# Kernel optimization log

Hardware: AMD Instinct MI355X
Metric: run time of the kernel (lower is better)

The kernel has to match this reference:

```python
import jax, jax.numpy as jnp
from jax import lax
import numpy as np

B, L = 16, 256
CHAR_SIZE, WORD_SIZE = 8000, 50000
EMB = 128            # char_embed (shared by char and word embeddings)
ENT_NUM, ENT_EMB = 30, 64
REL = 64             # rel_num
H = 10               # LSTM hidden (hard-coded in the source)


def lstm(x, mask, Wx, Wh, b, reverse=False):
    """Keras-style masked LSTM, return_sequences=True. x: [B,L,D], mask: [B,L] bool."""
    if reverse:
        x, mask = x[:, ::-1], mask[:, ::-1]
    gates_x = x @ Wx + b  # [B,L,4H] precomputed input projection

    def step(carry, inp):
        h, c = carry
        gx, m = inp  # gx: [B,4H], m: [B]
        z = gx + h @ Wh
        i, f, g, o = jnp.split(z, 4, axis=-1)  # keras gate order i,f,c,o
        i, f, o = jax.nn.sigmoid(i), jax.nn.sigmoid(f), jax.nn.sigmoid(o)
        c_new = f * c + i * jnp.tanh(g)
        h_new = o * jnp.tanh(c_new)
        m = m[:, None]
        h2 = jnp.where(m, h_new, h)  # masked steps carry previous state/output
        c2 = jnp.where(m, c_new, c)
        return (h2, c2), h2

    h0 = jnp.zeros((x.shape[0], Wh.shape[0]), x.dtype)
    _, hs = lax.scan(step, (h0, h0), (gates_x.transpose(1, 0, 2), mask.T))
    hs = hs.transpose(1, 0, 2)  # [B,L,H]
    if reverse:
        hs = hs[:, ::-1]
    return hs


def setup_inputs() -> dict:
    key = jax.random.key(0)
    ks = jax.random.split(key, 24)
    dense = lambda k, i, o: (0.05 * jax.random.normal(k, (i, o), jnp.float32))
    inp = {}
    inp["char_ids"] = jax.random.randint(ks[0], (B, L), 1, CHAR_SIZE, dtype=jnp.int32)
    inp["word_ids"] = jax.random.randint(ks[1], (B, L), 0, WORD_SIZE, dtype=jnp.int32)
    inp["entity_ids"] = jax.random.randint(ks[2], (B, L), 0, ENT_NUM, dtype=jnp.int32)
    inp["char_table"] = 0.05 * jax.random.normal(ks[3], (CHAR_SIZE, EMB), jnp.float32)
    inp["word_table"] = 0.05 * jax.random.normal(ks[4], (WORD_SIZE, EMB), jnp.float32)
    inp["ent_table"] = 0.05 * jax.random.normal(ks[5], (ENT_NUM, ENT_EMB), jnp.float32)
    D = 2 * EMB
    inp["Wx_f"], inp["Wh_f"], inp["b_f"] = dense(ks[6], D, 4 * H), dense(ks[7], H, 4 * H), jnp.zeros((4 * H,), jnp.float32)
    inp["Wx_b"], inp["Wh_b"], inp["b_b"] = dense(ks[8], D, 4 * H), dense(ks[9], H, 4 * H), jnp.zeros((4 * H,), jnp.float32)
    inp["We"], inp["be"] = dense(ks[10], 2 * H, ENT_NUM), jnp.zeros((ENT_NUM,), jnp.float32)
    ENC = 2 * H + ENT_EMB
    inp["Wu"], inp["bu"] = dense(ks[11], ENC, REL), jnp.zeros((REL,), jnp.float32)
    inp["Wv"], inp["bv"] = dense(ks[12], ENC, REL), jnp.zeros((REL,), jnp.float32)
    inp["Wuv"], inp["buv"] = dense(ks[13], 2 * REL, REL), jnp.zeros((REL,), jnp.float32)
    inp["Wr"], inp["br"] = dense(ks[14], REL, REL), jnp.zeros((REL,), jnp.float32)
    return inp


def reference(char_ids, word_ids, entity_ids, char_table, word_table, ent_table,
              Wx_f, Wh_f, b_f, Wx_b, Wh_b, b_b, We, be,
              Wu, bu, Wv, bv, Wuv, buv, Wr, br):
    mask = char_ids != 0  # [B,L]
    embed = jnp.concatenate([char_table[char_ids], word_table[word_ids]], axis=-1)  # [B,L,2E]
    h_fwd = lstm(embed, mask, Wx_f, Wh_f, b_f, reverse=False)
    h_bwd = lstm(embed, mask, Wx_b, Wh_b, b_b, reverse=True)
    sent = jnp.concatenate([h_fwd, h_bwd], axis=-1)  # [B,L,20]
    entity_logits = sent @ We + be  # [B,L,ENT_NUM]
    # training=True path: use gold entity_ids
    rel_enc = jnp.concatenate([sent, ent_table[entity_ids]], axis=-1)  # [B,L,ENC]
    su = jax.nn.relu(rel_enc @ Wu + bu)  # [B,L,REL]  (relu(tile(u)) == tile(relu(u)))
    sv = jax.nn.relu(rel_enc @ Wv + bv)  # [B,L,REL]
    # Dense over concat([u_tiled, v_tiled]) == split-weight matmul + broadcast add:
    # uv[b,i,j] = relu(su[b,j]) @ Wuv[:REL] + relu(sv[b,i]) @ Wuv[REL:] + buv
    A = jnp.einsum('bjr,rk->bjk', su, Wuv[:REL])  # depends on j (axis 2)
    C = jnp.einsum('bir,rk->bik', sv, Wuv[REL:])  # depends on i (axis 1)
    uv = A[:, None, :, :] + C[:, :, None, :] + buv  # [B,L,L,REL]
    rel_logits = jax.nn.softmax(uv @ Wr + br, axis=-1)  # [B,L,L,REL]
    return entity_logits, rel_logits
```

## Files before the change

kernel.cpp:

```cpp
#include <hip/hip_runtime.h>
#include <hip/hip_bf16.h>

#define Bb 16
#define Ll 256
#define EMBd 128
#define Hh 10
#define G4 40
#define ENTN 30
#define ENCd 84

__device__ __forceinline__ float ex2(float x){ return __builtin_amdgcn_exp2f(x); }
__device__ __forceinline__ float frcp(float x){ return __builtin_amdgcn_rcpf(x); }
#define LOG2E 1.4426950408889634f
__device__ __forceinline__ float sigf(float x){ return frcp(1.f + ex2(-LOG2E*x)); }
__device__ __forceinline__ float tanhf_fast(float x){ return 1.f - 2.f*frcp(1.f + ex2(2.f*LOG2E*x)); }

__global__ __launch_bounds__(256) void k0_weights(
    const float* __restrict__ Wuv, const float* __restrict__ buv,
    const float* __restrict__ Wr,  const float* __restrict__ br,
    float* __restrict__ W1, float* __restrict__ W2, float* __restrict__ biasp) {
  int idx = blockIdx.x*256 + threadIdx.x;
  if (idx < 4096) {
    int r = idx >> 6, k = idx & 63;
    float acc = 0.f;
    #pragma unroll 8
    for (int s = 0; s < 64; ++s) acc = fmaf(Wuv[r*64+s], Wr[s*64+k], acc);
    W1[idx] = acc;
  } else if (idx < 8192) {
    int j = idx - 4096; int r = j >> 6, k = j & 63;
    float acc = 0.f;
    #pragma unroll 8
    for (int s = 0; s < 64; ++s) acc = fmaf(Wuv[(64+r)*64+s], Wr[s*64+k], acc);
    W2[j] = acc;
  } else if (idx < 8256) {
    int k = idx - 8192;
    float acc = br[k];
    #pragma unroll 8
    for (int s = 0; s < 64; ++s) acc = fmaf(buv[s], Wr[s*64+k], acc);
    biasp[k] = acc;
  }
}

__global__ __launch_bounds__(128) void k1_embed_gates(
    const int* __restrict__ char_ids, const int* __restrict__ word_ids,
    const float* __restrict__ char_table, const float* __restrict__ word_table,
    const float* __restrict__ Wx_f, const float* __restrict__ b_f,
    const float* __restrict__ Wx_b, const float* __restrict__ b_b,
    float* __restrict__ gx_f, float* __restrict__ gx_b) {
  int tok = blockIdx.x;
  int b = tok >> 8, t = tok & 255;
  int tid = threadIdx.x;
  __shared__ float e[256];
  int cid = char_ids[tok];
  int wid = word_ids[tok];
  e[tid]       = char_table[cid*EMBd + tid];
  e[tid + 128] = word_table[wid*EMBd + tid];
  __syncthreads();
  if (tid < G4) {
    float acc = b_f[tid];
    #pragma unroll 8
    for (int k = 0; k < 256; ++k) acc = fmaf(e[k], Wx_f[k*G4 + tid], acc);
    gx_f[(t*Bb + b)*G4 + tid] = acc;
  } else if (tid >= 64 && tid < 64 + G4) {
    int u = tid - 64;
    float acc = b_b[u];
    #pragma unroll 8
    for (int k = 0; k < 256; ++k) acc = fmaf(e[k], Wx_b[k*G4 + u], acc);
    gx_b[((Ll-1-t)*Bb + b)*G4 + u] = acc;
  }
}

__global__ __launch_bounds__(64) void k2_lstm(
    const int* __restrict__ char_ids,
    const float* __restrict__ gx_f, const float* __restrict__ gx_b,
    const float* __restrict__ Wh_f, const float* __restrict__ Wh_b,
    float* __restrict__ sent) {
  int bid = blockIdx.x;
  int dir = bid & 1, b = bid >> 1;
  int lane = threadIdx.x;
  int j = lane < Hh ? lane : 0;
  const float* gx = dir ? gx_b : gx_f;
  const float* Wh = dir ? Wh_b : Wh_f;
  float wA[Hh], wB[Hh], wC[Hh], wD[Hh];
  #pragma unroll
  for (int k = 0; k < Hh; ++k) {
    wA[k] = Wh[k*G4 + j];
    wB[k] = Wh[k*G4 + j + Hh];
    wC[k] = Wh[k*G4 + j + 2*Hh];
    wD[k] = Wh[k*G4 + j + 3*Hh];
  }
  float hbc[Hh];
  #pragma unroll
  for (int k = 0; k < Hh; ++k) hbc[k] = 0.f;
  float c = 0.f, h = 0.f;
  const float* gp = gx + b*G4 + j;
  float nI = gp[0], nF = gp[Hh], nG = gp[2*Hh], nO = gp[3*Hh];
  int ncid = char_ids[b*Ll + (dir ? Ll-1 : 0)];
  for (int t = 0; t < Ll; ++t) {
    float gI = nI, gF = nF, gG = nG, gO = nO;
    int cid = ncid;
    if (t < Ll-1) {
      const float* gn = gp + (size_t)(t+1)*Bb*G4;
      nI = gn[0]; nF = gn[Hh]; nG = gn[2*Hh]; nO = gn[3*Hh];
      ncid = char_ids[b*Ll + (dir ? (Ll-2-t) : (t+1))];
    }
    float zi = gI, zf = gF, zg = gG, zo = gO;
    #pragma unroll
    for (int k = 0; k < Hh; ++k) {
      zi = fmaf(hbc[k], wA[k], zi);
      zf = fmaf(hbc[k], wB[k], zf);
      zg = fmaf(hbc[k], wC[k], zg);
      zo = fmaf(hbc[k], wD[k], zo);
    }
    float ig = sigf(zi), fg = sigf(zf), og = sigf(zo);
    float gg = tanhf_fast(zg);
    float cn = fmaf(fg, c, ig*gg);
    float hn = og * tanhf_fast(cn);
    bool m = (cid != 0);
    c = m ? cn : c;
    h = m ? hn : h;
    int t_orig = dir ? (Ll-1-t) : t;
    if (lane < Hh) sent[(b*Ll + t_orig)*20 + dir*Hh + lane] = h;
    #pragma unroll
    for (int k = 0; k < Hh; ++k)
      hbc[k] = __uint_as_float(__builtin_amdgcn_readlane(__float_as_uint(h), k));
  }
}

__global__ __launch_bounds__(64) void k3_token(
    const int* __restrict__ entity_ids,
    const float* __restrict__ ent_table,
    const float* __restrict__ sent,
    const float* __restrict__ We, const float* __restrict__ be,
    const float* __restrict__ Wu, const float* __restrict__ bu,
    const float* __restrict__ Wv, const float* __restrict__ bv,
    const float* __restrict__ W1, const float* __restrict__ W2,
    float* __restrict__ ent_logits, float* __restrict__ Ap, float* __restrict__ Cp) {
  int tok = blockIdx.x;
  int tid = threadIdx.x;
  __shared__ float enc[ENCd];
  __shared__ float su[64], sv[64];
  int eid = entity_ids[tok];
  if (tid < 20) enc[tid] = sent[tok*20 + tid];
  if (tid < ENCd - 20) enc[20 + tid] = ent_table[eid*64 + tid];
  __syncthreads();
  float a = bu[tid], v = bv[tid];
  #pragma unroll 4
  for (int k = 0; k < ENCd; ++k) {
    float ek = enc[k];
    a = fmaf(ek, Wu[k*64 + tid], a);
    v = fmaf(ek, Wv[k*64 + tid], v);
  }
  a = fmaxf(a, 0.f); v = fmaxf(v, 0.f);
  su[tid] = a; sv[tid] = v;
  if (tid < ENTN) {
    float el = be[tid];
    #pragma unroll
    for (int k = 0; k < 20; ++k) el = fmaf(enc[k], We[k*ENTN + tid], el);
    ent_logits[tok*ENTN + tid] = el;
  }
  __syncthreads();
  float accA = 0.f, accC = 0.f;
  #pragma unroll 8
  for (int r = 0; r < 64; ++r) {
    accA = fmaf(su[r], W1[r*64 + tid], accA);
    accC = fmaf(sv[r], W2[r*64 + tid], accC);
  }
  Ap[tok*64 + tid] = accA;
  Cp[tok*64 + tid] = accC;
}

__global__ __launch_bounds__(256) void k4_rel(
    const float* __restrict__ Ap, const float* __restrict__ Cp,
    const float* __restrict__ biasp, float* __restrict__ rel) {
  int tid = threadIdx.x;
  int rowLocal = tid >> 4;
  int k4 = tid & 15;
  int row = blockIdx.x*16 + rowLocal;
  int b  = row >> 16;
  int ij = row & 65535;
  int i  = ij >> 8, j = ij & 255;
  const float4 a4 = *(const float4*)(Ap + ((size_t)(b*Ll + j))*64 + k4*4);
  const float4 c4 = *(const float4*)(Cp + ((size_t)(b*Ll + i))*64 + k4*4);
  const float4 bb = *(const float4*)(biasp + k4*4);
  float x0 = a4.x + c4.x + bb.x;
  float x1 = a4.y + c4.y + bb.y;
  float x2 = a4.z + c4.z + bb.z;
  float x3 = a4.w + c4.w + bb.w;
  float m = fmaxf(fmaxf(x0, x1), fmaxf(x2, x3));
  #pragma unroll
  for (int s = 1; s < 16; s <<= 1) m = fmaxf(m, __shfl_xor(m, s));
  float e0 = ex2(LOG2E*(x0 - m));
  float e1 = ex2(LOG2E*(x1 - m));
  float e2 = ex2(LOG2E*(x2 - m));
  float e3 = ex2(LOG2E*(x3 - m));
  float ssum = (e0 + e1) + (e2 + e3);
  #pragma unroll
  for (int s = 1; s < 16; s <<= 1) ssum += __shfl_xor(ssum, s);
  float rs = frcp(ssum);
  float4 o; o.x = e0*rs; o.y = e1*rs; o.z = e2*rs; o.w = e3*rs;
  *(float4*)(rel + (size_t)row*64 + k4*4) = o;
}

extern "C" void kernel_launch(void* const* d_in, const int* in_sizes, int n_in,
                              void* d_out, int out_size, void* d_ws, size_t ws_size,
                              hipStream_t stream) {
  const int*   char_ids   = (const int*)  d_in[0];
  const int*   word_ids   = (const int*)  d_in[1];
  const int*   entity_ids = (const int*)  d_in[2];
  const float* char_table = (const float*)d_in[3];
  const float* word_table = (const float*)d_in[4];
  const float* ent_table  = (const float*)d_in[5];
  const float* Wx_f = (const float*)d_in[6];
  const float* Wh_f = (const float*)d_in[7];
  const float* b_f  = (const float*)d_in[8];
  const float* Wx_b = (const float*)d_in[9];
  const float* Wh_b = (const float*)d_in[10];
  const float* b_b  = (const float*)d_in[11];
  const float* We = (const float*)d_in[12];
  const float* be = (const float*)d_in[13];
  const float* Wu = (const float*)d_in[14];
  const float* bu = (const float*)d_in[15];
  const float* Wv = (const float*)d_in[16];
  const float* bv = (const float*)d_in[17];
  const float* Wuv = (const float*)d_in[18];
  const float* buv = (const float*)d_in[19];
  const float* Wr  = (const float*)d_in[20];
  const float* br  = (const float*)d_in[21];

  float* ws   = (float*)d_ws;
  float* gx_f = ws;
  float* gx_b = gx_f + 163840;
  float* sent = gx_b + 163840;
  float* W1   = sent + 81920;
  float* W2   = W1 + 4096;
  float* biasp= W2 + 4096;
  float* Ap   = biasp + 64;
  float* Cp   = Ap + 262144;

  float* out = (float*)d_out;
  float* ent_logits = out;
  float* rel = out + 122880;

  hipLaunchKernelGGL(k0_weights, dim3(33), dim3(256), 0, stream,
                     Wuv, buv, Wr, br, W1, W2, biasp);
  hipLaunchKernelGGL(k1_embed_gates, dim3(4096), dim3(128), 0, stream,
                     char_ids, word_ids, char_table, word_table,
                     Wx_f, b_f, Wx_b, b_b, gx_f, gx_b);
  hipLaunchKernelGGL(k2_lstm, dim3(32), dim3(64), 0, stream,
                     char_ids, gx_f, gx_b, Wh_f, Wh_b, sent);
  hipLaunchKernelGGL(k3_token, dim3(4096), dim3(64), 0, stream,
                     entity_ids, ent_table, sent, We, be, Wu, bu, Wv, bv,
                     W1, W2, ent_logits, Ap, Cp);
  hipLaunchKernelGGL(k4_rel, dim3(65536), dim3(256), 0, stream, Ap, Cp, biasp, rel);
}
```

Before: 164.7 us.

## Fuse weight precompute into embed kernel, lane-per-gate LSTM, batched token kernel, nontemporal stores

The weight-folding kernel is merged into the embedding/gate kernel as extra blocks, which removes one launch. The LSTM recurrence now gives one lane to each of the 40 gate outputs, computes activations with a select-based formula, and gathers the gates with ds_bpermute, which shortens the per-step dependency chain. The token kernel stages Wu/Wv in shared memory and processes 16 tokens per 256-thread block. The rel softmax output uses nontemporal stores to avoid cache pollution on the large write.

```diff
diff --git a/kernel.cpp b/kernel.cpp
--- a/kernel.cpp
+++ b/kernel.cpp
@@ -9,48 +9,50 @@
 #define ENTN 30
 #define ENCd 84
 
+typedef float f32x4 __attribute__((ext_vector_type(4)));
+
 __device__ __forceinline__ float ex2(float x){ return __builtin_amdgcn_exp2f(x); }
 __device__ __forceinline__ float frcp(float x){ return __builtin_amdgcn_rcpf(x); }
 #define LOG2E 1.4426950408889634f
 __device__ __forceinline__ float sigf(float x){ return frcp(1.f + ex2(-LOG2E*x)); }
 __device__ __forceinline__ float tanhf_fast(float x){ return 1.f - 2.f*frcp(1.f + ex2(2.f*LOG2E*x)); }
 
-__global__ __launch_bounds__(256) void k0_weights(
-    const float* __restrict__ Wuv, const float* __restrict__ buv,
-    const float* __restrict__ Wr,  const float* __restrict__ br,
-    float* __restrict__ W1, float* __restrict__ W2, float* __restrict__ biasp) {
-  int idx = blockIdx.x*256 + threadIdx.x;
-  if (idx < 4096) {
-    int r = idx >> 6, k = idx & 63;
-    float acc = 0.f;
-    #pragma unroll 8
-    for (int s = 0; s < 64; ++s) acc = fmaf(Wuv[r*64+s], Wr[s*64+k], acc);
-    W1[idx] = acc;
-  } else if (idx < 8192) {
-    int j = idx - 4096; int r = j >> 6, k = j & 63;
-    float acc = 0.f;
-    #pragma unroll 8
-    for (int s = 0; s < 64; ++s) acc = fmaf(Wuv[(64+r)*64+s], Wr[s*64+k], acc);
-    W2[j] = acc;
-  } else if (idx < 8256) {
-    int k = idx - 8192;
-    float acc = br[k];
-    #pragma unroll 8
-    for (int s = 0; s < 64; ++s) acc = fmaf(buv[s], Wr[s*64+k], acc);
-    biasp[k] = acc;
-  }
-}
-
-__global__ __launch_bounds__(128) void k1_embed_gates(
+__global__ __launch_bounds__(128) void k01_embed_gates_weights(
     const int* __restrict__ char_ids, const int* __restrict__ word_ids,
     const float* __restrict__ char_table, const float* __restrict__ word_table,
     const float* __restrict__ Wx_f, const float* __restrict__ b_f,
     const float* __restrict__ Wx_b, const float* __restrict__ b_b,
-    float* __restrict__ gx_f, float* __restrict__ gx_b) {
+    const float* __restrict__ Wuv, const float* __restrict__ buv,
+    const float* __restrict__ Wr,  const float* __restrict__ br,
+    float* __restrict__ gx_f, float* __restrict__ gx_b,
+    float* __restrict__ W1, float* __restrict__ W2, float* __restrict__ biasp) {
+  __shared__ float e[256];
+  if (blockIdx.x >= 4096) {
+    int idx = (blockIdx.x - 4096)*128 + threadIdx.x;
+    if (idx < 4096) {
+      int r = idx >> 6, k = idx & 63;
+      float acc = 0.f;
+      #pragma unroll 8
+      for (int s = 0; s < 64; ++s) acc = fmaf(Wuv[r*64+s], Wr[s*64+k], acc);
+      W1[idx] = acc;
+    } else if (idx < 8192) {
+      int jj = idx - 4096; int r = jj >> 6, k = jj & 63;
+      float acc = 0.f;
+      #pragma unroll 8
+      for (int s = 0; s < 64; ++s) acc = fmaf(Wuv[(64+r)*64+s], Wr[s*64+k], acc);
+      W2[jj] = acc;
+    } else if (idx < 8256) {
+      int k = idx - 8192;
+      float acc = br[k];
+      #pragma unroll 8
+      for (int s = 0; s < 64; ++s) acc = fmaf(buv[s], Wr[s*64+k], acc);
+      biasp[k] = acc;
+    }
+    return;
+  }
   int tok = blockIdx.x;
   int b = tok >> 8, t = tok & 255;
   int tid = threadIdx.x;
-  __shared__ float e[256];
   int cid = char_ids[tok];
   int wid = word_ids[tok];
   e[tid]       = char_table[cid*EMBd + tid];
@@ -78,56 +80,59 @@
   int bid = blockIdx.x;
   int dir = bid & 1, b = bid >> 1;
   int lane = threadIdx.x;
-  int j = lane < Hh ? lane : 0;
+  int l = lane < G4 ? lane : 0;
+  int g = (l >= 30) ? 3 : (l >= 20) ? 2 : (l >= 10) ? 1 : 0;
+  int j = l - 10*g;
   const float* gx = dir ? gx_b : gx_f;
   const float* Wh = dir ? Wh_b : Wh_f;
-  float wA[Hh], wB[Hh], wC[Hh], wD[Hh];
-  #pragma unroll
-  for (int k = 0; k < Hh; ++k) {
-    wA[k] = Wh[k*G4 + j];
-    wB[k] = Wh[k*G4 + j + Hh];
-    wC[k] = Wh[k*G4 + j + 2*Hh];
-    wD[k] = Wh[k*G4 + j + 3*Hh];
-  }
+  float w[Hh];
+  #pragma unroll
+  for (int k = 0; k < Hh; ++k) w[k] = Wh[k*G4 + l];
+  float s_    = (g == 2) ? (2.f*LOG2E) : (-LOG2E);
+  float a_    = (g == 2) ? 1.f : 0.f;
+  float bcoef = (g == 2) ? -2.f : 1.f;
+  float c = 0.f, h = 0.f;
   float hbc[Hh];
   #pragma unroll
   for (int k = 0; k < Hh; ++k) hbc[k] = 0.f;
-  float c = 0.f, h = 0.f;
-  const float* gp = gx + b*G4 + j;
-  float nI = gp[0], nF = gp[Hh], nG = gp[2*Hh], nO = gp[3*Hh];
-  int ncid = char_ids[b*Ll + (dir ? Ll-1 : 0)];
+  const int cbase = b*Ll;
+  float gnext = gx[(0*Bb + b)*G4 + l];
+  int ncid = char_ids[cbase + (dir ? Ll-1 : 0)];
   for (int t = 0; t < Ll; ++t) {
-    float gI = nI, gF = nF, gG = nG, gO = nO;
+    float gxv = gnext;
     int cid = ncid;
     if (t < Ll-1) {
-      const float* gn = gp + (size_t)(t+1)*Bb*G4;
-      nI = gn[0]; nF = gn[Hh]; nG = gn[2*Hh]; nO = gn[3*Hh];
-      ncid = char_ids[b*Ll + (dir ? (Ll-2-t) : (t+1))];
-    }
-    float zi = gI, zf = gF, zg = gG, zo = gO;
+      gnext = gx[((t+1)*Bb + b)*G4 + l];
+      ncid = char_ids[cbase + (dir ? (Ll-2-t) : (t+1))];
+    }
+    float z0 = gxv, z1 = 0.f;
     #pragma unroll
-    for (int k = 0; k < Hh; ++k) {
-      zi = fmaf(hbc[k], wA[k], zi);
-      zf = fmaf(hbc[k], wB[k], zf);
-      zg = fmaf(hbc[k], wC[k], zg);
-      zo = fmaf(hbc[k], wD[k], zo);
-    }
-    float ig = sigf(zi), fg = sigf(zf), og = sigf(zo);
-    float gg = tanhf_fast(zg);
-    float cn = fmaf(fg, c, ig*gg);
-    float hn = og * tanhf_fast(cn);
+    for (int k = 0; k < Hh; k += 2) {
+      z0 = fmaf(hbc[k],   w[k],   z0);
+      z1 = fmaf(hbc[k+1], w[k+1], z1);
+    }
+    float z = z0 + z1;
+    float tt  = frcp(1.f + ex2(s_*z));
+    float act = fmaf(bcoef, tt, a_);
+    int ib = __float_as_int(act);
+    float iv = __int_as_float(__builtin_amdgcn_ds_bpermute((j       )*4, ib));
+    float fv = __int_as_float(__builtin_amdgcn_ds_bpermute((Hh   + j)*4, ib));
+    float gv = __int_as_float(__builtin_amdgcn_ds_bpermute((2*Hh + j)*4, ib));
+    float ov = __int_as_float(__builtin_amdgcn_ds_bpermute((3*Hh + j)*4, ib));
+    float cn = fmaf(fv, c, iv*gv);
+    float hn = ov * tanhf_fast(cn);
     bool m = (cid != 0);
     c = m ? cn : c;
     h = m ? hn : h;
     int t_orig = dir ? (Ll-1-t) : t;
-    if (lane < Hh) sent[(b*Ll + t_orig)*20 + dir*Hh + lane] = h;
+    if (lane < Hh) sent[(cbase + t_orig)*20 + dir*Hh + lane] = h;
     #pragma unroll
     for (int k = 0; k < Hh; ++k)
       hbc[k] = __uint_as_float(__builtin_amdgcn_readlane(__float_as_uint(h), k));
   }
 }
 
-__global__ __launch_bounds__(64) void k3_token(
+__global__ __launch_bounds__(256) void k3_token(
     const int* __restrict__ entity_ids,
     const float* __restrict__ ent_table,
     const float* __restrict__ sent,
@@ -136,38 +141,52 @@
     const float* __restrict__ Wv, const float* __restrict__ bv,
     const float* __restrict__ W1, const float* __restrict__ W2,
     float* __restrict__ ent_logits, float* __restrict__ Ap, float* __restrict__ Cp) {
-  int tok = blockIdx.x;
+  __shared__ float sWu[ENCd*64];
+  __shared__ float sWv[ENCd*64];
+  __shared__ float encs[4][ENCd];
+  __shared__ float sus[4][64];
+  __shared__ float svs[4][64];
   int tid = threadIdx.x;
-  __shared__ float enc[ENCd];
-  __shared__ float su[64], sv[64];
-  int eid = entity_ids[tok];
-  if (tid < 20) enc[tid] = sent[tok*20 + tid];
-  if (tid < ENCd - 20) enc[20 + tid] = ent_table[eid*64 + tid];
+  for (int idx = tid; idx < ENCd*64; idx += 256) {
+    sWu[idx] = Wu[idx];
+    sWv[idx] = Wv[idx];
+  }
+  int wave = tid >> 6, lane = tid & 63;
+  int tok0 = blockIdx.x * 16 + wave * 4;
+  float bu_l = bu[lane], bv_l = bv[lane];
   __syncthreads();
-  float a = bu[tid], v = bv[tid];
-  #pragma unroll 4
-  for (int k = 0; k < ENCd; ++k) {
-    float ek = enc[k];
-    a = fmaf(ek, Wu[k*64 + tid], a);
-    v = fmaf(ek, Wv[k*64 + tid], v);
-  }
-  a = fmaxf(a, 0.f); v = fmaxf(v, 0.f);
-  su[tid] = a; sv[tid] = v;
-  if (tid < ENTN) {
-    float el = be[tid];
-    #pragma unroll
-    for (int k = 0; k < 20; ++k) el = fmaf(enc[k], We[k*ENTN + tid], el);
-    ent_logits[tok*ENTN + tid] = el;
-  }
-  __syncthreads();
-  float accA = 0.f, accC = 0.f;
-  #pragma unroll 8
-  for (int r = 0; r < 64; ++r) {
-    accA = fmaf(su[r], W1[r*64 + tid], accA);
-    accC = fmaf(sv[r], W2[r*64 + tid], accC);
-  }
-  Ap[tok*64 + tid] = accA;
-  Cp[tok*64 + tid] = accC;
+  for (int it = 0; it < 4; ++it) {
+    int tok = tok0 + it;
+    int eid = entity_ids[tok];
+    if (lane < 20) encs[wave][lane] = sent[tok*20 + lane];
+    encs[wave][20 + lane] = ent_table[eid*64 + lane];
+    __syncthreads();
+    float a = bu_l, v = bv_l;
+    #pragma unroll 4
+    for (int k = 0; k < ENCd; ++k) {
+      float ek = encs[wave][k];
+      a = fmaf(ek, sWu[k*64 + lane], a);
+      v = fmaf(ek, sWv[k*64 + lane], v);
+    }
+    a = fmaxf(a, 0.f); v = fmaxf(v, 0.f);
+    sus[wave][lane] = a; svs[wave][lane] = v;
+    if (lane < ENTN) {
+      float el = be[lane];
+      #pragma unroll
+      for (int k = 0; k < 20; ++k) el = fmaf(encs[wave][k], We[k*ENTN + lane], el);
+      ent_logits[tok*ENTN + lane] = el;
+    }
+    __syncthreads();
+    float accA = 0.f, accC = 0.f;
+    #pragma unroll 8
+    for (int r = 0; r < 64; ++r) {
+      accA = fmaf(sus[wave][r], W1[r*64 + lane], accA);
+      accC = fmaf(svs[wave][r], W2[r*64 + lane], accC);
+    }
+    Ap[tok*64 + lane] = accA;
+    Cp[tok*64 + lane] = accC;
+    __syncthreads();
+  }
 }
 
 __global__ __launch_bounds__(256) void k4_rel(
@@ -180,9 +199,9 @@
   int b  = row >> 16;
   int ij = row & 65535;
   int i  = ij >> 8, j = ij & 255;
-  const float4 a4 = *(const float4*)(Ap + ((size_t)(b*Ll + j))*64 + k4*4);
-  const float4 c4 = *(const float4*)(Cp + ((size_t)(b*Ll + i))*64 + k4*4);
-  const float4 bb = *(const float4*)(biasp + k4*4);
+  const f32x4 a4 = *(const f32x4*)(Ap + ((size_t)(b*Ll + j))*64 + k4*4);
+  const f32x4 c4 = *(const f32x4*)(Cp + ((size_t)(b*Ll + i))*64 + k4*4);
+  const f32x4 bb = *(const f32x4*)(biasp + k4*4);
   float x0 = a4.x + c4.x + bb.x;
   float x1 = a4.y + c4.y + bb.y;
   float x2 = a4.z + c4.z + bb.z;
@@ -198,8 +217,8 @@
   #pragma unroll
   for (int s = 1; s < 16; s <<= 1) ssum += __shfl_xor(ssum, s);
   float rs = frcp(ssum);
-  float4 o; o.x = e0*rs; o.y = e1*rs; o.z = e2*rs; o.w = e3*rs;
-  *(float4*)(rel + (size_t)row*64 + k4*4) = o;
+  f32x4 o; o.x = e0*rs; o.y = e1*rs; o.z = e2*rs; o.w = e3*rs;
+  __builtin_nontemporal_store(o, (f32x4*)(rel + (size_t)row*64 + k4*4));
 }
 
 extern "C" void kernel_launch(void* const* d_in, const int* in_sizes, int n_in,
@@ -242,14 +261,13 @@
   float* ent_logits = out;
   float* rel = out + 122880;
 
-  hipLaunchKernelGGL(k0_weights, dim3(33), dim3(256), 0, stream,
-                     Wuv, buv, Wr, br, W1, W2, biasp);
-  hipLaunchKernelGGL(k1_embed_gates, dim3(4096), dim3(128), 0, stream,
+  hipLaunchKernelGGL(k01_embed_gates_weights, dim3(4162), dim3(128), 0, stream,
                      char_ids, word_ids, char_table, word_table,
-                     Wx_f, b_f, Wx_b, b_b, gx_f, gx_b);
+                     Wx_f, b_f, Wx_b, b_b, Wuv, buv, Wr, br,
+                     gx_f, gx_b, W1, W2, biasp);
   hipLaunchKernelGGL(k2_lstm, dim3(32), dim3(64), 0, stream,
                      char_ids, gx_f, gx_b, Wh_f, Wh_b, sent);
-  hipLaunchKernelGGL(k3_token, dim3(4096), dim3(64), 0, stream,
+  hipLaunchKernelGGL(k3_token, dim3(256), dim3(256), 0, stream,
                      entity_ids, ent_table, sent, We, be, Wu, bu, Wv, bv,
                      W1, W2, ent_logits, Ap, Cp);
   hipLaunchKernelGGL(k4_rel, dim3(65536), dim3(256), 0, stream, Ap, Cp, biasp, rel);
```

Result: faster. 153.5 us (-6.8%).
